# Optimization experiments

Hardware: AMD Instinct MI355X
Metric: run time of the kernel (lower is better)

The kernel has to match this reference:

```python
import jax, jax.numpy as jnp
import numpy as np

IN_DIM = 1024
OUT_DIM = 1024
HIDDEN = 1024
T = 16384
R_MIN, R_MAX, MAX_PHASE = 0.9, 0.999, 6.28


@jax.vmap
def binary_operator_diag(q_i, q_j):
    A_i, b_i = q_i
    A_j, b_j = q_j
    return (A_j * A_i, A_j * b_i + b_j)


def setup_inputs() -> dict:
    key = jax.random.key(0)
    ks = jax.random.split(key, 8)
    inputs = jax.random.normal(ks[0], (T, IN_DIM), dtype=jnp.float32)
    # nu_log / theta_log per original initializers
    u1 = jax.random.uniform(ks[1], (HIDDEN,), dtype=jnp.float32)
    nu_log = jnp.log(-0.5 * jnp.log(u1 * (R_MAX ** 2 - R_MIN ** 2) + R_MIN ** 2))
    u2 = jax.random.uniform(ks[2], (HIDDEN,), dtype=jnp.float32)
    theta_log = jnp.log(MAX_PHASE * u2)
    diag_lambda = jnp.exp(-jnp.exp(nu_log) + 1j * jnp.exp(theta_log))
    gamma_log = jnp.log(jnp.sqrt(1 - jnp.abs(diag_lambda) ** 2))
    B_re = jax.random.normal(ks[3], (IN_DIM, HIDDEN), dtype=jnp.float32) / jnp.sqrt(2.0 * IN_DIM)
    B_im = jax.random.normal(ks[4], (IN_DIM, HIDDEN), dtype=jnp.float32) / jnp.sqrt(2.0 * IN_DIM)
    C_re = jax.random.normal(ks[5], (OUT_DIM, HIDDEN), dtype=jnp.float32) / jnp.sqrt(1.0 * HIDDEN)
    C_im = jax.random.normal(ks[6], (OUT_DIM, HIDDEN), dtype=jnp.float32) / jnp.sqrt(1.0 * HIDDEN)
    D = jax.random.normal(ks[7], (OUT_DIM, IN_DIM), dtype=jnp.float32)
    return {"inputs": inputs, "nu_log": nu_log, "theta_log": theta_log,
            "gamma_log": gamma_log, "B_re": B_re, "B_im": B_im,
            "C_re": C_re, "C_im": C_im, "D": D}


def reference(inputs, nu_log, theta_log, gamma_log, B_re, B_im, C_re, C_im, D):
    # diagonal complex transition eigenvalues, shape (H,)
    diag_lambda = jnp.exp(-jnp.exp(nu_log) + 1j * jnp.exp(theta_log))
    # NOTE: original code expands gamma on axis=-1 -> (H, 1); broadcasts against
    # B_norm (in_dim, H) because in_dim == hidden_dim. Reproduced faithfully.
    B_norm = (B_re + 1j * B_im) * jnp.exp(gamma_log)[:, None]
    C = C_re + 1j * C_im
    T_len = inputs.shape[-2]
    Lambda_elements = jnp.repeat(diag_lambda[None, :], T_len, axis=0)  # (T, H)
    Bu_elements = jnp.einsum('ih,ti->th', B_norm, inputs)              # (T, H) complex
    _, hidden_states = jax.lax.associative_scan(
        binary_operator_diag, (Lambda_elements, Bu_elements))
    outputs = jnp.real(jnp.einsum('th,oh->to', hidden_states, C))      # (T, out)
    outputs = outputs + jnp.einsum('ti,io->to', inputs, D)             # D used as 'io'
    return outputs
```

## Files before the change

kernel.cpp:

```cpp
#include <hip/hip_runtime.h>
#include <hip/hip_bf16.h>
#include <stdint.h>

#define T_LEN   16384
#define HID     1024
#define KDIM    1024
#define CHUNK   64
#define NCHUNK  256

typedef __bf16 bf16x8 __attribute__((ext_vector_type(8)));
typedef float  f32x4  __attribute__((ext_vector_type(4)));

__device__ inline ushort f2bf(float f) {
  union { float f; uint32_t u; } v; v.f = f;
  uint32_t r = v.u + 0x7FFF + ((v.u >> 16) & 1);
  return (ushort)(r >> 16);
}
__device__ inline float bf2f(ushort u) {
  union { uint32_t u; float f; } v; v.u = ((uint32_t)u) << 16;
  return v.f;
}

__device__ inline void gload16(const void* g, void* l) {
  __builtin_amdgcn_global_load_lds(
      (const __attribute__((address_space(1))) void*)g,
      (__attribute__((address_space(3))) void*)l, 16, 0, 0);
}

__global__ __launch_bounds__(256) void prep_kernel(
    const float* __restrict__ nu_log, const float* __restrict__ theta_log,
    const float* __restrict__ gamma_log,
    float* __restrict__ lam_re, float* __restrict__ lam_im, float* __restrict__ eg) {
  int h = blockIdx.x * 256 + threadIdx.x;
  if (h < HID) {
    float mag = expf(-expf(nu_log[h]));
    float th  = expf(theta_log[h]);
    lam_re[h] = mag * cosf(th);
    lam_im[h] = mag * sinf(th);
    eg[h]     = expf(gamma_log[h]);
  }
}

__global__ __launch_bounds__(256) void convX(
    const float* __restrict__ src, ushort* __restrict__ dst) {
  size_t i = ((size_t)blockIdx.x * 256 + threadIdx.x) * 4;
  float4 v = *(const float4*)(src + i);
  ushort4 o;
  o.x = f2bf(v.x); o.y = f2bf(v.y); o.z = f2bf(v.z); o.w = f2bf(v.w);
  *(ushort4*)(dst + i) = o;
}

__global__ __launch_bounds__(256) void weight_prep(
    const float* __restrict__ Bre, const float* __restrict__ Bim,
    const float* __restrict__ Cre, const float* __restrict__ Cim,
    const float* __restrict__ D,   const float* __restrict__ eg,
    ushort* __restrict__ BreT, ushort* __restrict__ BimT,
    ushort* __restrict__ CreB, ushort* __restrict__ CimB,
    ushort* __restrict__ DT) {
  __shared__ float tile[32][33];
  int z = blockIdx.z;
  if (z == 2 || z == 3) {
    const float* src = (z == 2) ? Cre : Cim;
    ushort* dst = (z == 2) ? CreB : CimB;
    float s = (z == 2) ? 1.0f : -1.0f;
    size_t base = ((size_t)blockIdx.y * 32 + (threadIdx.x >> 3)) * 1024 +
                  blockIdx.x * 32 + (threadIdx.x & 7) * 4;
    float4 v = *(const float4*)(src + base);
    ushort4 o;
    o.x = f2bf(v.x * s); o.y = f2bf(v.y * s);
    o.z = f2bf(v.z * s); o.w = f2bf(v.w * s);
    *(ushort4*)(dst + base) = o;
    return;
  }
  const float* src = (z == 0) ? Bre : (z == 1) ? Bim : D;
  ushort* dst = (z == 0) ? BreT : (z == 1) ? BimT : DT;
  bool scaled = (z < 2);
  int bx = blockIdx.x * 32;
  int by = blockIdx.y * 32;
  int tx = threadIdx.x & 31, ty = threadIdx.x >> 5;
#pragma unroll
  for (int r = 0; r < 32; r += 8)
    tile[ty + r][tx] = src[(size_t)(by + ty + r) * 1024 + bx + tx];
  __syncthreads();
  float sc = scaled ? eg[by + tx] : 1.0f;
#pragma unroll
  for (int r = 0; r < 32; r += 8)
    dst[(size_t)(bx + ty + r) * 1024 + by + tx] = f2bf(tile[tx][ty + r] * sc);
}

__device__ __forceinline__ void gemm_accum(
    const ushort* __restrict__ A, int lda, const ushort* __restrict__ B,
    ushort* As, ushort* Bs, int tb, int nb, f32x4 acc[4][4]) {
  const int tid = threadIdx.x;
  const int w = tid >> 6, l = tid & 63;
  const int wrow = w & 1, wcol = w >> 1;
  const int lo = l & 15, q = l >> 4;
  const int rs = l >> 2;
  const int cs = (l & 3) * 8;
  for (int k0 = 0; k0 < KDIM; k0 += 32) {
#pragma unroll
    for (int i = 0; i < 2; ++i) {
      int win = w * 2 + i;
      int r = win * 16 + rs;
      gload16(A + (size_t)(tb + r) * lda + k0 + cs, As + win * 512);
      gload16(B + (size_t)(nb + r) * KDIM + k0 + cs, Bs + win * 512);
    }
    __syncthreads();
    bf16x8 af[4], bfr[4];
#pragma unroll
    for (int i = 0; i < 4; ++i) {
      af[i]  = *(const bf16x8*)(As + (wrow * 64 + i * 16 + lo) * 32 + q * 8);
      bfr[i] = *(const bf16x8*)(Bs + (wcol * 64 + i * 16 + lo) * 32 + q * 8);
    }
#pragma unroll
    for (int i = 0; i < 4; ++i)
#pragma unroll
      for (int j = 0; j < 4; ++j)
        acc[i][j] = __builtin_amdgcn_mfma_f32_16x16x32_bf16(af[i], bfr[j], acc[i][j], 0, 0, 0);
    __syncthreads();
  }
}

__global__ __launch_bounds__(256) void gemm_bu(
    const ushort* __restrict__ A, const ushort* __restrict__ B,
    ushort* __restrict__ O) {
  __shared__ __align__(16) ushort As[4096], Bs[4096];
  f32x4 acc[4][4];
#pragma unroll
  for (int i = 0; i < 4; ++i)
#pragma unroll
    for (int j = 0; j < 4; ++j) acc[i][j] = (f32x4){0.f, 0.f, 0.f, 0.f};
  int tb = blockIdx.x * 128, nb = blockIdx.y * 128;
  gemm_accum(A, KDIM, B, As, Bs, tb, nb, acc);
  const int tid = threadIdx.x;
  const int w = tid >> 6, l = tid & 63;
  const int wrow = w & 1, wcol = w >> 1;
  const int lo = l & 15, q = l >> 4;
#pragma unroll
  for (int i = 0; i < 4; ++i)
#pragma unroll
    for (int j = 0; j < 4; ++j) {
      int col = nb + wcol * 64 + j * 16 + lo;
#pragma unroll
      for (int r = 0; r < 4; ++r) {
        int row = tb + wrow * 64 + i * 16 + q * 4 + r;
        O[(size_t)row * 2048 + col] = f2bf(acc[i][j][r]);
      }
    }
}

__global__ __launch_bounds__(256) void gemm3(
    const ushort* __restrict__ Hall,
    const ushort* __restrict__ CreB, const ushort* __restrict__ CimB,
    const ushort* __restrict__ X,    const ushort* __restrict__ DT,
    float* __restrict__ O) {
  __shared__ __align__(16) ushort As[4096], Bs[4096];
  f32x4 acc[4][4];
#pragma unroll
  for (int i = 0; i < 4; ++i)
#pragma unroll
    for (int j = 0; j < 4; ++j) acc[i][j] = (f32x4){0.f, 0.f, 0.f, 0.f};
  int tb = blockIdx.x * 128, nb = blockIdx.y * 128;
  gemm_accum(Hall,        2048, CreB, As, Bs, tb, nb, acc);
  gemm_accum(Hall + 1024, 2048, CimB, As, Bs, tb, nb, acc);
  gemm_accum(X,           1024, DT,   As, Bs, tb, nb, acc);
  const int tid = threadIdx.x;
  const int w = tid >> 6, l = tid & 63;
  const int wrow = w & 1, wcol = w >> 1;
  const int lo = l & 15, q = l >> 4;
#pragma unroll
  for (int i = 0; i < 4; ++i)
#pragma unroll
    for (int j = 0; j < 4; ++j) {
      int col = nb + wcol * 64 + j * 16 + lo;
#pragma unroll
      for (int r = 0; r < 4; ++r) {
        int row = tb + wrow * 64 + i * 16 + q * 4 + r;
        O[(size_t)row * HID + col] = acc[i][j][r];
      }
    }
}

__global__ __launch_bounds__(256) void scan_sums(
    const ushort* __restrict__ Bu,
    const float* __restrict__ lam_re, const float* __restrict__ lam_im,
    float* __restrict__ Sre, float* __restrict__ Sim) {
  int h0 = (blockIdx.y * 256 + threadIdx.x) * 2;
  int c = blockIdx.x;
  float lr0 = lam_re[h0], li0 = lam_im[h0];
  float lr1 = lam_re[h0 + 1], li1 = lam_im[h0 + 1];
  float hr0 = 0.f, hi0 = 0.f, hr1 = 0.f, hi1 = 0.f;
  const uint* P = (const uint*)Bu;
  size_t baseR = (size_t)c * CHUNK * 1024 + (h0 >> 1);
  size_t baseI = baseR + 512;
#pragma unroll 8
  for (int t = 0; t < CHUNK; ++t) {
    uint re = P[baseR + (size_t)t * 1024];
    uint im = P[baseI + (size_t)t * 1024];
    float br0 = bf2f((ushort)re), br1 = bf2f((ushort)(re >> 16));
    float bi0 = bf2f((ushort)im), bi1 = bf2f((ushort)(im >> 16));
    float nr0 = fmaf(lr0, hr0, fmaf(-li0, hi0, br0));
    float ni0 = fmaf(lr0, hi0, fmaf(li0, hr0, bi0));
    float nr1 = fmaf(lr1, hr1, fmaf(-li1, hi1, br1));
    float ni1 = fmaf(lr1, hi1, fmaf(li1, hr1, bi1));
    hr0 = nr0; hi0 = ni0; hr1 = nr1; hi1 = ni1;
  }
  Sre[(size_t)c * HID + h0] = hr0;  Sre[(size_t)c * HID + h0 + 1] = hr1;
  Sim[(size_t)c * HID + h0] = hi0;  Sim[(size_t)c * HID + h0 + 1] = hi1;
}

__global__ __launch_bounds__(256) void scan_carry(
    const float* __restrict__ Sre, const float* __restrict__ Sim,
    const float* __restrict__ lam_re, const float* __restrict__ lam_im,
    float* __restrict__ Pre, float* __restrict__ Pim) {
  int h = blockIdx.x * 256 + threadIdx.x;
  float lr = lam_re[h], li = lam_im[h];
  float pr = lr, pi = li;
#pragma unroll
  for (int s = 0; s < 6; ++s) {
    float nr = pr * pr - pi * pi;
    float ni = 2.f * pr * pi;
    pr = nr; pi = ni;
  }
  float cr = 0.f, ci = 0.f;
  for (int c = 0; c < NCHUNK; ++c) {
    Pre[(size_t)c * HID + h] = cr;
    Pim[(size_t)c * HID + h] = ci;
    float sr = Sre[(size_t)c * HID + h];
    float si = Sim[(size_t)c * HID + h];
    float nr = fmaf(pr, cr, fmaf(-pi, ci, sr));
    float ni = fmaf(pr, ci, fmaf(pi, cr, si));
    cr = nr; ci = ni;
  }
}

__global__ __launch_bounds__(256) void scan_emit(
    const ushort* __restrict__ Bu,
    const float* __restrict__ lam_re, const float* __restrict__ lam_im,
    const float* __restrict__ Pre, const float* __restrict__ Pim,
    ushort* __restrict__ Hall) {
  int h0 = (blockIdx.y * 256 + threadIdx.x) * 2;
  int c = blockIdx.x;
  float lr0 = lam_re[h0], li0 = lam_im[h0];
  float lr1 = lam_re[h0 + 1], li1 = lam_im[h0 + 1];
  float hr0 = Pre[(size_t)c * HID + h0], hi0 = Pim[(size_t)c * HID + h0];
  float hr1 = Pre[(size_t)c * HID + h0 + 1], hi1 = Pim[(size_t)c * HID + h0 + 1];
  const uint* P = (const uint*)Bu;
  uint* Q = (uint*)Hall;
  size_t baseR = (size_t)c * CHUNK * 1024 + (h0 >> 1);
  size_t baseI = baseR + 512;
#pragma unroll 8
  for (int t = 0; t < CHUNK; ++t) {
    uint re = P[baseR + (size_t)t * 1024];
    uint im = P[baseI + (size_t)t * 1024];
    float br0 = bf2f((ushort)re), br1 = bf2f((ushort)(re >> 16));
    float bi0 = bf2f((ushort)im), bi1 = bf2f((ushort)(im >> 16));
    float nr0 = fmaf(lr0, hr0, fmaf(-li0, hi0, br0));
    float ni0 = fmaf(lr0, hi0, fmaf(li0, hr0, bi0));
    float nr1 = fmaf(lr1, hr1, fmaf(-li1, hi1, br1));
    float ni1 = fmaf(lr1, hi1, fmaf(li1, hr1, bi1));
    hr0 = nr0; hi0 = ni0; hr1 = nr1; hi1 = ni1;
    Q[baseR + (size_t)t * 1024] = (uint)f2bf(hr0) | ((uint)f2bf(hr1) << 16);
    Q[baseI + (size_t)t * 1024] = (uint)f2bf(hi0) | ((uint)f2bf(hi1) << 16);
  }
}

extern "C" void kernel_launch(void* const* d_in, const int* in_sizes, int n_in,
                              void* d_out, int out_size, void* d_ws, size_t ws_size,
                              hipStream_t stream) {
  const float* inputs    = (const float*)d_in[0];
  const float* nu_log    = (const float*)d_in[1];
  const float* theta_log = (const float*)d_in[2];
  const float* gamma_log = (const float*)d_in[3];
  const float* B_re      = (const float*)d_in[4];
  const float* B_im      = (const float*)d_in[5];
  const float* C_re      = (const float*)d_in[6];
  const float* C_im      = (const float*)d_in[7];
  const float* D         = (const float*)d_in[8];
  float* out = (float*)d_out;

  char* ws = (char*)d_ws;
  constexpr size_t TH = (size_t)T_LEN * HID;
  constexpr size_t W  = (size_t)1024 * 1024;
  constexpr size_t CH = (size_t)NCHUNK * HID;

  ushort* Xbf  = (ushort*)(ws);
  ushort* Bu   = (ushort*)(ws + TH * 2);
  ushort* Hall = (ushort*)(ws + TH * 6);
  char*   p    = ws + TH * 10;
  ushort* Ball = (ushort*)(p);             p += 2 * W * 2;
  ushort* CreB = (ushort*)(p);             p += W * 2;
  ushort* CimB = (ushort*)(p);             p += W * 2;
  ushort* DT   = (ushort*)(p);             p += W * 2;
  float*  Sre  = (float*)(p);              p += CH * 4;
  float*  Sim  = (float*)(p);              p += CH * 4;
  float*  Pre  = (float*)(p);              p += CH * 4;
  float*  Pim  = (float*)(p);              p += CH * 4;
  float*  lamR = (float*)(p);              p += 4096;
  float*  lamI = (float*)(p);              p += 4096;
  float*  eg   = (float*)(p);              p += 4096;
  ushort* BreT = Ball;
  ushort* BimT = Ball + W;

  prep_kernel<<<dim3(HID / 256), 256, 0, stream>>>(nu_log, theta_log, gamma_log,
                                                   lamR, lamI, eg);
  convX<<<dim3((unsigned)(TH / 4 / 256)), 256, 0, stream>>>(inputs, Xbf);
  weight_prep<<<dim3(32, 32, 5), 256, 0, stream>>>(B_re, B_im, C_re, C_im, D, eg,
                                                   BreT, BimT, CreB, CimB, DT);

  gemm_bu<<<dim3(T_LEN / 128, 2048 / 128), 256, 0, stream>>>(Xbf, Ball, Bu);

  scan_sums<<<dim3(NCHUNK, HID / 512), 256, 0, stream>>>(Bu, lamR, lamI, Sre, Sim);
  scan_carry<<<dim3(HID / 256), 256, 0, stream>>>(Sre, Sim, lamR, lamI, Pre, Pim);
  scan_emit<<<dim3(NCHUNK, HID / 512), 256, 0, stream>>>(Bu, lamR, lamI, Pre, Pim,
                                                         Hall);

  gemm3<<<dim3(T_LEN / 128, HID / 128), 256, 0, stream>>>(Hall, CreB, CimB, Xbf, DT,
                                                          out);
}
```

Before: 410.3 us.

## Rewrite GEMMs as 256x256 double-buffered, swizzled, pipelined MFMA kernels

Replaces the simple 128x128, 256-thread GEMM loop with a 256x256 tile, 512-thread kernel. It double-buffers the A and B tiles in LDS with XOR-swizzled columns, interleaves global-to-LDS loads with MFMA quarters using explicit waitcnt and barrier scheduling, and remaps block IDs for L2 locality. The aim is to hide memory latency, raise arithmetic intensity and cut LDS bank conflicts in both the Bu projection and the output GEMM. In exchange it uses 128KB of LDS per block, heavy register pressure from 32 accumulators, and many barriers. The larger tiles also give fewer workgroups (512 and 256 blocks).

Measured after the change: 361.6 us. 1.13x faster.

```diff
diff --git a/kernel.cpp b/kernel.cpp
--- a/kernel.cpp
+++ b/kernel.cpp
@@ -88,96 +88,175 @@
     dst[(size_t)(bx + ty + r) * 1024 + by + tx] = f2bf(tile[tx][ty + r] * sc);
 }
 
-__device__ __forceinline__ void gemm_accum(
+
+#define BAR()   __builtin_amdgcn_s_barrier()
+#define SCH0()  __builtin_amdgcn_sched_barrier(0)
+#define LGKM0() asm volatile("s_waitcnt lgkmcnt(0)")
+#define VM4()   asm volatile("s_waitcnt vmcnt(4)")
+#define VM0()   asm volatile("s_waitcnt vmcnt(0)")
+
+#define STAGE_HALF(G, LDA, R0, K0, LT, HALF)                         \
+  do {                                                               \
+    _Pragma("unroll")                                                \
+    for (int is_ = 0; is_ < 2; ++is_) {                              \
+      int seg_ = w * 2 + is_;                                        \
+      int gr_ = (R0) + (HALF) * 128 + seg_ * 8 + (l >> 3);           \
+      int gc_ = (K0) + (((l & 7) ^ (l >> 3)) << 3);                  \
+      gload16((G) + (size_t)gr_ * (LDA) + gc_,                       \
+              (LT) + (HALF) * 8192 + seg_ * 512);                    \
+    }                                                                \
+  } while (0)
+
+#define DS_A(QM, BUF)                                                \
+  do {                                                               \
+    _Pragma("unroll")                                                \
+    for (int m_ = 0; m_ < 4; ++m_) {                                 \
+      int r_ = (wr * 128 + ((QM) * 4 + m_) * 16 + lo) * 64;          \
+      a[m_][0] = *(const bf16x8*)((BUF) + r_ + c0us);                \
+      a[m_][1] = *(const bf16x8*)((BUF) + r_ + c1us);                \
+    }                                                                \
+  } while (0)
+
+#define DS_B(QN, BUF, REG)                                           \
+  do {                                                               \
+    _Pragma("unroll")                                                \
+    for (int n_ = 0; n_ < 2; ++n_) {                                 \
+      int r_ = (wc * 64 + ((QN) * 2 + n_) * 16 + lo) * 64;           \
+      REG[n_][0] = *(const bf16x8*)((BUF) + r_ + c0us);              \
+      REG[n_][1] = *(const bf16x8*)((BUF) + r_ + c1us);              \
+    }                                                                \
+  } while (0)
+
+#define MFMA_Q(QM, QN, REG)                                          \
+  do {                                                               \
+    __builtin_amdgcn_s_setprio(1);                                   \
+    _Pragma("unroll")                                                \
+    for (int m_ = 0; m_ < 4; ++m_)                                   \
+      _Pragma("unroll")                                              \
+      for (int n_ = 0; n_ < 2; ++n_) {                               \
+        f32x4* ac_ = &acc[(QM) * 4 + m_][(QN) * 2 + n_];             \
+        *ac_ = __builtin_amdgcn_mfma_f32_16x16x32_bf16(              \
+            a[m_][0], REG[n_][0], *ac_, 0, 0, 0);                    \
+        *ac_ = __builtin_amdgcn_mfma_f32_16x16x32_bf16(              \
+            a[m_][1], REG[n_][1], *ac_, 0, 0, 0);                    \
+      }                                                              \
+    __builtin_amdgcn_s_setprio(0);                                   \
+  } while (0)
+
+__device__ __forceinline__ void gemm256_seg(
     const ushort* __restrict__ A, int lda, const ushort* __restrict__ B,
-    ushort* As, ushort* Bs, int tb, int nb, f32x4 acc[4][4]) {
+    ushort* lds, int row0, int col0,
+    int w, int l, int wr, int wc, int lo, int q, int c0us, int c1us,
+    f32x4 acc[8][4]) {
+  ushort* A0 = lds;
+  ushort* A1 = lds + 16384;
+  ushort* B0 = lds + 32768;
+  ushort* B1 = lds + 49152;
+  bf16x8 a[4][2], bq0[2][2], bq1[2][2];
+  STAGE_HALF(A, lda, row0, 0, A0, 0);
+  STAGE_HALF(A, lda, row0, 0, A0, 1);
+  STAGE_HALF(B, 1024, col0, 0, B0, 0);
+  STAGE_HALF(B, 1024, col0, 0, B0, 1);
+  STAGE_HALF(B, 1024, col0, 64, B1, 0);
+  STAGE_HALF(B, 1024, col0, 64, B1, 1);
+  VM4(); BAR(); SCH0();
+  for (int i = 0; i < 8; ++i) {
+    const int k1 = (2 * i + 1) * 64;
+    const int k2 = (2 * i + 2) * 64;
+    const int k3 = (2 * i + 3) * 64;
+    const bool st2 = (i < 7);
+    DS_A(0, A0); DS_B(0, B0, bq0);
+    STAGE_HALF(A, lda, row0, k1, A1, 0);
+    BAR(); LGKM0(); SCH0(); MFMA_Q(0, 0, bq0); BAR(); SCH0();
+    DS_B(1, B0, bq1);
+    STAGE_HALF(A, lda, row0, k1, A1, 1);
+    BAR(); LGKM0(); SCH0(); MFMA_Q(0, 1, bq1); BAR(); SCH0();
+    DS_A(1, A0);
+    if (st2) STAGE_HALF(B, 1024, col0, k2, B0, 0);
+    BAR(); LGKM0(); SCH0(); MFMA_Q(1, 0, bq0); BAR(); SCH0();
+    if (st2) { STAGE_HALF(B, 1024, col0, k2, B0, 1); VM4(); } else { VM0(); }
+    BAR(); LGKM0(); SCH0(); MFMA_Q(1, 1, bq1); BAR(); SCH0();
+    DS_A(0, A1); DS_B(0, B1, bq0);
+    if (st2) STAGE_HALF(A, lda, row0, k2, A0, 0);
+    BAR(); LGKM0(); SCH0(); MFMA_Q(0, 0, bq0); BAR(); SCH0();
+    DS_B(1, B1, bq1);
+    if (st2) STAGE_HALF(A, lda, row0, k2, A0, 1);
+    BAR(); LGKM0(); SCH0(); MFMA_Q(0, 1, bq1); BAR(); SCH0();
+    DS_A(1, A1);
+    if (st2) STAGE_HALF(B, 1024, col0, k3, B1, 0);
+    BAR(); LGKM0(); SCH0(); MFMA_Q(1, 0, bq0); BAR(); SCH0();
+    if (st2) { STAGE_HALF(B, 1024, col0, k3, B1, 1); VM4(); } else { VM0(); }
+    BAR(); LGKM0(); SCH0(); MFMA_Q(1, 1, bq1); BAR(); SCH0();
+  }
+}
+
+__global__ __launch_bounds__(512, 2) void gemm_bu(
+    const ushort* __restrict__ A, const ushort* __restrict__ B,
+    ushort* __restrict__ O) {
+  __shared__ __align__(16) ushort lds[65536];
   const int tid = threadIdx.x;
   const int w = tid >> 6, l = tid & 63;
-  const int wrow = w & 1, wcol = w >> 1;
+  const int wr = w >> 2, wc = w & 3;
   const int lo = l & 15, q = l >> 4;
-  const int rs = l >> 2;
-  const int cs = (l & 3) * 8;
-  for (int k0 = 0; k0 < KDIM; k0 += 32) {
-#pragma unroll
-    for (int i = 0; i < 2; ++i) {
-      int win = w * 2 + i;
-      int r = win * 16 + rs;
-      gload16(A + (size_t)(tb + r) * lda + k0 + cs, As + win * 512);
-      gload16(B + (size_t)(nb + r) * KDIM + k0 + cs, Bs + win * 512);
+  const int xorv = (lo & 7) << 4;
+  const int c0us = ((q * 16) ^ xorv) >> 1;
+  const int c1us = ((64 + q * 16) ^ xorv) >> 1;
+  const int id = blockIdx.y * 64 + blockIdx.x;
+  const int nwg = 64 * (int)gridDim.y;
+  const int s = (id & 7) * (nwg >> 3) + (id >> 3);
+  const int row0 = (s & 63) * 256, col0 = (s >> 6) * 256;
+  f32x4 acc[8][4];
+#pragma unroll
+  for (int m = 0; m < 8; ++m)
+#pragma unroll
+    for (int n = 0; n < 4; ++n) acc[m][n] = (f32x4){0.f, 0.f, 0.f, 0.f};
+  gemm256_seg(A, 1024, B, lds, row0, col0, w, l, wr, wc, lo, q, c0us, c1us, acc);
+  const int rowb = row0 + wr * 128, colb = col0 + wc * 64;
+#pragma unroll
+  for (int m = 0; m < 8; ++m)
+#pragma unroll
+    for (int n = 0; n < 4; ++n) {
+      int col = colb + n * 16 + lo;
+#pragma unroll
+      for (int r = 0; r < 4; ++r)
+        O[(size_t)(rowb + m * 16 + q * 4 + r) * 2048 + col] = f2bf(acc[m][n][r]);
     }
-    __syncthreads();
-    bf16x8 af[4], bfr[4];
-#pragma unroll
-    for (int i = 0; i < 4; ++i) {
-      af[i]  = *(const bf16x8*)(As + (wrow * 64 + i * 16 + lo) * 32 + q * 8);
-      bfr[i] = *(const bf16x8*)(Bs + (wcol * 64 + i * 16 + lo) * 32 + q * 8);
-    }
-#pragma unroll
-    for (int i = 0; i < 4; ++i)
-#pragma unroll
-      for (int j = 0; j < 4; ++j)
-        acc[i][j] = __builtin_amdgcn_mfma_f32_16x16x32_bf16(af[i], bfr[j], acc[i][j], 0, 0, 0);
-    __syncthreads();
-  }
-}
-
-__global__ __launch_bounds__(256) void gemm_bu(
-    const ushort* __restrict__ A, const ushort* __restrict__ B,
-    ushort* __restrict__ O) {
-  __shared__ __align__(16) ushort As[4096], Bs[4096];
-  f32x4 acc[4][4];
-#pragma unroll
-  for (int i = 0; i < 4; ++i)
-#pragma unroll
-    for (int j = 0; j < 4; ++j) acc[i][j] = (f32x4){0.f, 0.f, 0.f, 0.f};
-  int tb = blockIdx.x * 128, nb = blockIdx.y * 128;
-  gemm_accum(A, KDIM, B, As, Bs, tb, nb, acc);
-  const int tid = threadIdx.x;
-  const int w = tid >> 6, l = tid & 63;
-  const int wrow = w & 1, wcol = w >> 1;
-  const int lo = l & 15, q = l >> 4;
-#pragma unroll
-  for (int i = 0; i < 4; ++i)
-#pragma unroll
-    for (int j = 0; j < 4; ++j) {
-      int col = nb + wcol * 64 + j * 16 + lo;
-#pragma unroll
-      for (int r = 0; r < 4; ++r) {
-        int row = tb + wrow * 64 + i * 16 + q * 4 + r;
-        O[(size_t)row * 2048 + col] = f2bf(acc[i][j][r]);
-      }
-    }
-}
-
-__global__ __launch_bounds__(256) void gemm3(
+}
+
+__global__ __launch_bounds__(512, 2) void gemm3(
     const ushort* __restrict__ Hall,
     const ushort* __restrict__ CreB, const ushort* __restrict__ CimB,
     const ushort* __restrict__ X,    const ushort* __restrict__ DT,
     float* __restrict__ O) {
-  __shared__ __align__(16) ushort As[4096], Bs[4096];
-  f32x4 acc[4][4];
-#pragma unroll
-  for (int i = 0; i < 4; ++i)
-#pragma unroll
-    for (int j = 0; j < 4; ++j) acc[i][j] = (f32x4){0.f, 0.f, 0.f, 0.f};
-  int tb = blockIdx.x * 128, nb = blockIdx.y * 128;
-  gemm_accum(Hall,        2048, CreB, As, Bs, tb, nb, acc);
-  gemm_accum(Hall + 1024, 2048, CimB, As, Bs, tb, nb, acc);
-  gemm_accum(X,           1024, DT,   As, Bs, tb, nb, acc);
+  __shared__ __align__(16) ushort lds[65536];
   const int tid = threadIdx.x;
   const int w = tid >> 6, l = tid & 63;
-  const int wrow = w & 1, wcol = w >> 1;
+  const int wr = w >> 2, wc = w & 3;
   const int lo = l & 15, q = l >> 4;
-#pragma unroll
-  for (int i = 0; i < 4; ++i)
-#pragma unroll
-    for (int j = 0; j < 4; ++j) {
-      int col = nb + wcol * 64 + j * 16 + lo;
-#pragma unroll
-      for (int r = 0; r < 4; ++r) {
-        int row = tb + wrow * 64 + i * 16 + q * 4 + r;
-        O[(size_t)row * HID + col] = acc[i][j][r];
-      }
+  const int xorv = (lo & 7) << 4;
+  const int c0us = ((q * 16) ^ xorv) >> 1;
+  const int c1us = ((64 + q * 16) ^ xorv) >> 1;
+  const int id = blockIdx.y * 64 + blockIdx.x;
+  const int nwg = 64 * (int)gridDim.y;
+  const int s = (id & 7) * (nwg >> 3) + (id >> 3);
+  const int row0 = (s & 63) * 256, col0 = (s >> 6) * 256;
+  f32x4 acc[8][4];
+#pragma unroll
+  for (int m = 0; m < 8; ++m)
+#pragma unroll
+    for (int n = 0; n < 4; ++n) acc[m][n] = (f32x4){0.f, 0.f, 0.f, 0.f};
+  gemm256_seg(Hall,        2048, CreB, lds, row0, col0, w, l, wr, wc, lo, q, c0us, c1us, acc);
+  gemm256_seg(Hall + 1024, 2048, CimB, lds, row0, col0, w, l, wr, wc, lo, q, c0us, c1us, acc);
+  gemm256_seg(X,           1024, DT,   lds, row0, col0, w, l, wr, wc, lo, q, c0us, c1us, acc);
+  const int rowb = row0 + wr * 128, colb = col0 + wc * 64;
+#pragma unroll
+  for (int m = 0; m < 8; ++m)
+#pragma unroll
+    for (int n = 0; n < 4; ++n) {
+      int col = colb + n * 16 + lo;
+#pragma unroll
+      for (int r = 0; r < 4; ++r)
+        O[(size_t)(rowb + m * 16 + q * 4 + r) * HID + col] = acc[m][n][r];
     }
 }
 
@@ -308,13 +387,13 @@
   weight_prep<<<dim3(32, 32, 5), 256, 0, stream>>>(B_re, B_im, C_re, C_im, D, eg,
                                                    BreT, BimT, CreB, CimB, DT);
 
-  gemm_bu<<<dim3(T_LEN / 128, 2048 / 128), 256, 0, stream>>>(Xbf, Ball, Bu);
+  gemm_bu<<<dim3(T_LEN / 256, 2048 / 256), 512, 0, stream>>>(Xbf, Ball, Bu);
 
   scan_sums<<<dim3(NCHUNK, HID / 512), 256, 0, stream>>>(Bu, lamR, lamI, Sre, Sim);
   scan_carry<<<dim3(HID / 256), 256, 0, stream>>>(Sre, Sim, lamR, lamI, Pre, Pim);
   scan_emit<<<dim3(NCHUNK, HID / 512), 256, 0, stream>>>(Bu, lamR, lamI, Pre, Pim,
                                                          Hall);
 
-  gemm3<<<dim3(T_LEN / 128, HID / 128), 256, 0, stream>>>(Hall, CreB, CimB, Xbf, DT,
+  gemm3<<<dim3(T_LEN / 256, HID / 256), 512, 0, stream>>>(Hall, CreB, CimB, Xbf, DT,
                                                           out);
 }
```
